# Kernel optimization log

Measured on AMD Instinct MI355X. Metric: run time of the kernel, lower is better.

## Reference

```python
import jax, jax.numpy as jnp
import numpy as np


def setup_inputs() -> dict:
    key = jax.random.key(0)
    ks = jax.random.split(key, 6)
    B, Lq, Lk, D = 8, 2048, 2048, 128
    return {
        "query": jax.random.normal(ks[0], (B, Lq, D), dtype=jnp.float32),
        "x": jax.random.normal(ks[1], (B, Lk, D), dtype=jnp.float32),
        "valid": jax.random.randint(ks[2], (B, Lq, Lk), 0, 2, dtype=jnp.int32),
        "Wq": jax.random.normal(ks[3], (D, D), dtype=jnp.float32) * 0.05,
        "Wk": jax.random.normal(ks[4], (D, D), dtype=jnp.float32) * 0.05,
        "Wv": jax.random.normal(ks[5], (D, D), dtype=jnp.float32) * 0.05,
    }


def reference(query, x, valid, Wq, Wk, Wv):
    # bias-free linear projections; torch Linear weight is [out, in] -> y = x @ W.T
    q = jnp.einsum("bqd,ad->bqa", query, Wq)   # [B, Lq, D]
    k = jnp.einsum("bkd,ad->bka", x, Wk)        # [B, Lk, D]
    v = jnp.einsum("bkd,ad->bka", x, Wv)        # [B, Lk, D]
    # scores (no scale arg passed in this config)
    att = jnp.einsum("bqd,bkd->bqk", q, k)      # [B, Lq, Lk]
    # max-subtraction BEFORE masking (matches original op order)
    att = att - jnp.max(att, axis=-1, keepdims=True)
    att = jnp.where(valid <= 0, -jnp.inf, att)
    att_w = jax.nn.softmax(att, axis=-1)
    # rows with all entries masked produce NaN -> fill with 0
    att_w = jnp.where(jnp.isnan(att_w), jnp.zeros_like(att_w), att_w)
    result = jnp.einsum("bqk,bkd->bqd", att_w, v)
    return (result, att_w)
```

## Files before the change

kernel.cpp:

```cpp
#include <hip/hip_runtime.h>
#include <float.h>
#include <math.h>


#define BB 8
#define LQ 2048
#define LK 2048
#define DD 128
#define NROWS (BB*LQ)
#define KS 4

typedef __attribute__((ext_vector_type(8))) _Float16 half8;
typedef __attribute__((ext_vector_type(8))) unsigned short ushort8;
typedef __attribute__((ext_vector_type(4))) float f32x4;

#define QH_OFF  (0u)
#define QL_OFF  (1u*NROWS*DD*2u)
#define KH_OFF  (2u*NROWS*DD*2u)
#define KL_OFF  (3u*NROWS*DD*2u)
#define VTH_OFF (4u*NROWS*DD*2u)
#define VTL_OFF (5u*NROWS*DD*2u)
#define BM_OFF  (6u*NROWS*DD*2u)
#define MZ_OFF  (BM_OFF + (unsigned)NROWS*(LK/8))

__device__ __forceinline__ f32x4 mfma16(half8 a, half8 b, f32x4 c) {
  return __builtin_amdgcn_mfma_f32_16x16x32_f16(a, b, c, 0, 0, 0);
}

__global__ __launch_bounds__(256, 3) void proj_kernel(
    const float* __restrict__ query, const float* __restrict__ x,
    const float* __restrict__ Wq, const float* __restrict__ Wk,
    const float* __restrict__ Wv, unsigned char* __restrict__ wsb)
{
  __shared__ float SB[8704];
  const int which = blockIdx.y;
  const float* __restrict__ src = (which == 0) ? query : x;
  const float* __restrict__ W   = (which == 0) ? Wq : (which == 1 ? Wk : Wv);
  const int t = threadIdx.x, l = t & 63, wv = t >> 6;
  const int lr = l & 15, lg = l >> 4;
  const int r0 = blockIdx.x * 64;

#pragma unroll
  for (int j = 0; j < 8; ++j) {
    const int flat = j * 1024 + t * 4;
    const int row = flat >> 7, col = flat & 127;
    *(float4*)&SB[row * 132 + col] = *(const float4*)&src[(size_t)(r0 + row) * DD + col];
  }
  __syncthreads();

  half8 ah[4], al[4];
#pragma unroll
  for (int dc = 0; dc < 4; ++dc) {
    const int base = (wv * 16 + lr) * 132 + dc * 32 + lg * 8;
    float4 f0 = *(const float4*)&SB[base];
    float4 f1 = *(const float4*)&SB[base + 4];
    float f[8] = {f0.x, f0.y, f0.z, f0.w, f1.x, f1.y, f1.z, f1.w};
#pragma unroll
    for (int e = 0; e < 8; ++e) {
      _Float16 h = (_Float16)f[e];
      ah[dc][e] = h;
      al[dc][e] = (_Float16)(f[e] - (float)h);
    }
  }
  __syncthreads();

  f32x4 acc[8];
#pragma unroll
  for (int a = 0; a < 8; ++a) acc[a] = (f32x4){0.f, 0.f, 0.f, 0.f};

#pragma unroll
  for (int dc = 0; dc < 4; ++dc) {
#pragma unroll
    for (int a = 0; a < 8; ++a) {
      const float* p = W + (size_t)(a * 16 + lr) * DD + dc * 32 + lg * 8;
      float4 f0 = *(const float4*)p;
      float4 f1 = *(const float4*)(p + 4);
      float f[8] = {f0.x, f0.y, f0.z, f0.w, f1.x, f1.y, f1.z, f1.w};
      half8 bh, bl;
#pragma unroll
      for (int e = 0; e < 8; ++e) {
        _Float16 h = (_Float16)f[e];
        bh[e] = h;
        bl[e] = (_Float16)(f[e] - (float)h);
      }
      acc[a] = mfma16(ah[dc], bh, acc[a]);
      acc[a] = mfma16(al[dc], bh, acc[a]);
      acc[a] = mfma16(ah[dc], bl, acc[a]);
    }
  }

  if (which < 2) {
    _Float16* Oh = (_Float16*)(wsb + (which == 0 ? QH_OFF : KH_OFF));
    _Float16* Ol = (_Float16*)(wsb + (which == 0 ? QL_OFF : KL_OFF));
#pragma unroll
    for (int a = 0; a < 8; ++a)
#pragma unroll
      for (int i = 0; i < 4; ++i) {
        const int ro = r0 + wv * 16 + lg * 4 + i;
        const int co = a * 16 + lr;
        float v = acc[a][i];
        _Float16 h = (_Float16)v;
        Oh[(size_t)ro * DD + co] = h;
        Ol[(size_t)ro * DD + co] = (_Float16)(v - (float)h);
      }
  } else {
    _Float16* TH = (_Float16*)SB;
    _Float16* TL = TH + 8704;
#pragma unroll
    for (int a = 0; a < 8; ++a)
#pragma unroll
      for (int i = 0; i < 4; ++i) {
        const int rl = wv * 16 + lg * 4 + i;
        const int co = a * 16 + lr;
        float v = acc[a][i];
        _Float16 h = (_Float16)v;
        TH[co * 68 + rl] = h;
        TL[co * 68 + rl] = (_Float16)(v - (float)h);
      }
    __syncthreads();
    _Float16* Vh = (_Float16*)(wsb + VTH_OFF);
    _Float16* Vl = (_Float16*)(wsb + VTL_OFF);
    const int b = r0 >> 11, kloc = r0 & 2047;
    const int d = t >> 1, hh = t & 1;
    const size_t gb = ((size_t)(b * DD + d)) * LK + kloc + hh * 32;
#pragma unroll
    for (int j = 0; j < 8; ++j) {
      *(ushort4*)(Vh + gb + j * 4) = *(const ushort4*)&TH[d * 68 + hh * 32 + j * 4];
      *(ushort4*)(Vl + gb + j * 4) = *(const ushort4*)&TL[d * 68 + hh * 32 + j * 4];
    }
  }
}

__global__ __launch_bounds__(256) void maskpack_kernel(
    const int* __restrict__ valid, unsigned long long* __restrict__ bm)
{
  const int t = threadIdx.x, l = t & 63, wv = t >> 6;
  const size_t base = (size_t)blockIdx.x * 32768 + (size_t)wv * 8192;
  for (int it = 0; it < 32; ++it) {
    int v0 = valid[base + (size_t)(it * 4 + 0) * 64 + l];
    int v1 = valid[base + (size_t)(it * 4 + 1) * 64 + l];
    int v2 = valid[base + (size_t)(it * 4 + 2) * 64 + l];
    int v3 = valid[base + (size_t)(it * 4 + 3) * 64 + l];
    unsigned long long m0 = __ballot(v0 > 0);
    unsigned long long m1 = __ballot(v1 > 0);
    unsigned long long m2 = __ballot(v2 > 0);
    unsigned long long m3 = __ballot(v3 > 0);
    if (l == 0) {
      bm[(base >> 6) + it * 4 + 0] = m0;
      bm[(base >> 6) + it * 4 + 1] = m1;
      bm[(base >> 6) + it * 4 + 2] = m2;
      bm[(base >> 6) + it * 4 + 3] = m3;
    }
  }
}

__global__ __launch_bounds__(256, 4) void scores_kernel(
    const unsigned char* __restrict__ wsb, float* __restrict__ att)
{
  __shared__ unsigned short KHs[64 * 136];
  __shared__ unsigned short KLs[64 * 136];
  const int t = threadIdx.x, l = t & 63, wv = t >> 6;
  const int lr = l & 15, lg = l >> 4;
  const int qb = blockIdx.x, b = blockIdx.y, ks = blockIdx.z;
  const int rowg = b * LQ + qb * 64;
  const int kbase = ks * 512;
  const _Float16* QH = (const _Float16*)(wsb + QH_OFF);
  const _Float16* QL = (const _Float16*)(wsb + QL_OFF);
  const _Float16* KH = (const _Float16*)(wsb + KH_OFF);
  const _Float16* KL = (const _Float16*)(wsb + KL_OFF);
  const unsigned* bm32 = (const unsigned*)(wsb + BM_OFF);
  float* M = (float*)(wsb + MZ_OFF);
  float* Z = M + KS * NROWS;

  half8 qh[4], ql[4];
#pragma unroll
  for (int dc = 0; dc < 4; ++dc) {
    const size_t idx = ((size_t)(rowg + wv * 16 + lr)) * DD + dc * 32 + lg * 8;
    qh[dc] = *(const half8*)(QH + idx);
    ql[dc] = *(const half8*)(QL + idx);
  }

  ushort8 rh[4], rl[4];
  auto issue_stage = [&](int kt) {
#pragma unroll
    for (int j = 0; j < 4; ++j) {
      const int flat = j * 2048 + t * 8;
      const int row = flat >> 7, col = flat & 127;
      const size_t g = ((size_t)(b * LK + kbase + kt * 64 + row)) * DD + col;
      rh[j] = *(const ushort8*)(KH + g);
      rl[j] = *(const ushort8*)(KL + g);
    }
  };
  auto write_stage = [&]() {
#pragma unroll
    for (int j = 0; j < 4; ++j) {
      const int flat = j * 2048 + t * 8;
      const int row = flat >> 7, col = flat & 127;
      *(ushort8*)&KHs[row * 136 + col] = rh[j];
      *(ushort8*)&KLs[row * 136 + col] = rl[j];
    }
  };

  issue_stage(0);
  write_stage();

  float m_run[4], z_run[4];
#pragma unroll
  for (int i = 0; i < 4; ++i) { m_run[i] = -FLT_MAX; z_run[i] = 0.f; }

  for (int kt = 0; kt < 8; ++kt) {
    const int k0 = kbase + kt * 64;
    if (kt < 7) issue_stage(kt + 1);
    unsigned mw0[4], mw1[4];
#pragma unroll
    for (int i = 0; i < 4; ++i) {
      uint2 u = *(const uint2*)(bm32 + ((size_t)(rowg + wv * 16 + lg * 4 + i)) * 64 + (k0 >> 5));
      mw0[i] = u.x; mw1[i] = u.y;
    }
    __syncthreads();

    f32x4 acc[4];
#pragma unroll
    for (int kg = 0; kg < 4; ++kg) acc[kg] = (f32x4){0.f, 0.f, 0.f, 0.f};
#pragma unroll
    for (int kg = 0; kg < 4; ++kg)
#pragma unroll
      for (int dc = 0; dc < 4; ++dc) {
        half8 bh = *(const half8*)&KHs[(kg * 16 + lr) * 136 + dc * 32 + lg * 8];
        half8 bl = *(const half8*)&KLs[(kg * 16 + lr) * 136 + dc * 32 + lg * 8];
        acc[kg] = mfma16(qh[dc], bh, acc[kg]);
        acc[kg] = mfma16(ql[dc], bh, acc[kg]);
        acc[kg] = mfma16(qh[dc], bl, acc[kg]);
      }

#pragma unroll
    for (int i = 0; i < 4; ++i) {
      float sv[4];
      float* ap = att + ((size_t)(rowg + wv * 16 + lg * 4 + i)) * LK + k0 + lr;
#pragma unroll
      for (int kg = 0; kg < 4; ++kg) {
        unsigned w = (kg < 2) ? mw0[i] : mw1[i];
        int bit = (w >> (((kg & 1) * 16) + lr)) & 1;
        float v = bit ? acc[kg][i] : -INFINITY;
        sv[kg] = v;
        ap[kg * 16] = v;
      }
      float tm = fmaxf(fmaxf(sv[0], sv[1]), fmaxf(sv[2], sv[3]));
#pragma unroll
      for (int o = 1; o < 16; o <<= 1) tm = fmaxf(tm, __shfl_xor(tm, o));
      const float mo = m_run[i], mn = fmaxf(mo, tm);
      float za = __expf(sv[0] - mn) + __expf(sv[1] - mn) +
                 __expf(sv[2] - mn) + __expf(sv[3] - mn);
      z_run[i] = z_run[i] * __expf(mo - mn) + za;
      m_run[i] = mn;
    }
    __syncthreads();
    if (kt < 7) write_stage();
  }

#pragma unroll
  for (int i = 0; i < 4; ++i) {
    float z = z_run[i];
#pragma unroll
    for (int o = 1; o < 16; o <<= 1) z += __shfl_xor(z, o);
    if (lr == 0) {
      const size_t row = (size_t)(rowg + wv * 16 + lg * 4 + i);
      M[(size_t)ks * NROWS + row] = m_run[i];
      Z[(size_t)ks * NROWS + row] = z;
    }
  }
}

__global__ __launch_bounds__(256, 3) void pv_kernel(
    const unsigned char* __restrict__ wsb, float* __restrict__ att,
    float* __restrict__ res)
{
  __shared__ float Ws[64 * 68];
  __shared__ unsigned short VHs[128 * 72];
  __shared__ unsigned short VLs[128 * 72];
  const int t = threadIdx.x, l = t & 63, wv = t >> 6;
  const int lr = l & 15, lg = l >> 4;
  const int qb = blockIdx.x, b = blockIdx.y, kp = blockIdx.z;
  const int rowg = b * LQ + qb * 64;
  const int kbase = kp * 512;
  const _Float16* VTH = (const _Float16*)(wsb + VTH_OFF);
  const _Float16* VTL = (const _Float16*)(wsb + VTL_OFF);
  const float* M = (const float*)(wsb + MZ_OFF);
  const float* Z = M + KS * NROWS;

  const int srow = t >> 2, scb = (t & 3) * 16;
  float mg, zi;
  {
    const size_t row = (size_t)(rowg + srow);
    float m0 = M[row], m1 = M[NROWS + row], m2 = M[2 * NROWS + row], m3 = M[3 * NROWS + row];
    mg = fmaxf(fmaxf(m0, m1), fmaxf(m2, m3));
    float z = Z[row] * __expf(m0 - mg) + Z[NROWS + row] * __expf(m1 - mg) +
              Z[2 * NROWS + row] * __expf(m2 - mg) + Z[3 * NROWS + row] * __expf(m3 - mg);
    zi = (z > 0.f) ? 1.f / z : 0.f;
  }

  ushort8 vhr[4], vlr[4];
  float4 sr[4];
  auto issue_V = [&](int kt) {
#pragma unroll
    for (int j = 0; j < 4; ++j) {
      const int flat = j * 2048 + t * 8;
      const int d = flat >> 6, kk = flat & 63;
      const size_t g = ((size_t)(b * DD + d)) * LK + kbase + kt * 64 + kk;
      vhr[j] = *(const ushort8*)(VTH + g);
      vlr[j] = *(const ushort8*)(VTL + g);
    }
  };
  auto issue_S = [&](int kt) {
    const size_t rb = (size_t)(rowg + srow) * LK + kbase + kt * 64 + scb;
#pragma unroll
    for (int j = 0; j < 4; ++j) sr[j] = *(const float4*)&att[rb + j * 4];
  };
  auto wcompute_write = [&](int kt) {
    const size_t rb = (size_t)(rowg + srow) * LK + kbase + kt * 64 + scb;
#pragma unroll
    for (int j = 0; j < 4; ++j) {
      float4 w4;
      w4.x = __expf(sr[j].x - mg) * zi;
      w4.y = __expf(sr[j].y - mg) * zi;
      w4.z = __expf(sr[j].z - mg) * zi;
      w4.w = __expf(sr[j].w - mg) * zi;
      *(float4*)&Ws[srow * 68 + scb + j * 4] = w4;
      *(float4*)&att[rb + j * 4] = w4;
    }
#pragma unroll
    for (int j = 0; j < 4; ++j) {
      const int flat = j * 2048 + t * 8;
      const int d = flat >> 6, kk = flat & 63;
      *(ushort8*)&VHs[d * 72 + kk] = vhr[j];
      *(ushort8*)&VLs[d * 72 + kk] = vlr[j];
    }
  };

  f32x4 oacc[8];
#pragma unroll
  for (int df = 0; df < 8; ++df) oacc[df] = (f32x4){0.f, 0.f, 0.f, 0.f};

  issue_V(0); issue_S(0);
  wcompute_write(0);

  for (int kt = 0; kt < 8; ++kt) {
    if (kt < 7) { issue_V(kt + 1); issue_S(kt + 1); }
    __syncthreads();

#pragma unroll
    for (int kc = 0; kc < 2; ++kc) {
      const int abase = (wv * 16 + lr) * 68 + kc * 32 + lg * 8;
      float4 a0 = *(const float4*)&Ws[abase];
      float4 a1 = *(const float4*)&Ws[abase + 4];
      half8 wf;
      wf[0] = (_Float16)a0.x; wf[1] = (_Float16)a0.y;
      wf[2] = (_Float16)a0.z; wf[3] = (_Float16)a0.w;
      wf[4] = (_Float16)a1.x; wf[5] = (_Float16)a1.y;
      wf[6] = (_Float16)a1.z; wf[7] = (_Float16)a1.w;
#pragma unroll
      for (int df = 0; df < 8; ++df) {
        half8 vh = *(const half8*)&VHs[(df * 16 + lr) * 72 + kc * 32 + lg * 8];
        half8 vl = *(const half8*)&VLs[(df * 16 + lr) * 72 + kc * 32 + lg * 8];
        oacc[df] = mfma16(wf, vh, oacc[df]);
        oacc[df] = mfma16(wf, vl, oacc[df]);
      }
    }
    __syncthreads();
    if (kt < 7) wcompute_write(kt + 1);
  }

#pragma unroll
  for (int df = 0; df < 8; ++df)
#pragma unroll
    for (int i = 0; i < 4; ++i)
      atomicAdd(&res[((size_t)(rowg + wv * 16 + lg * 4 + i)) * DD + df * 16 + lr],
                oacc[df][i]);
}

extern "C" void kernel_launch(void* const* d_in, const int* in_sizes, int n_in,
                              void* d_out, int out_size, void* d_ws, size_t ws_size,
                              hipStream_t stream)
{
  (void)in_sizes; (void)n_in; (void)out_size; (void)ws_size;
  const float* query = (const float*)d_in[0];
  const float* x     = (const float*)d_in[1];
  const int*   valid = (const int*)d_in[2];
  const float* Wq    = (const float*)d_in[3];
  const float* Wk    = (const float*)d_in[4];
  const float* Wv    = (const float*)d_in[5];

  float* out = (float*)d_out;
  float* res = out;
  float* att = out + (size_t)NROWS * DD;
  unsigned char* wsb = (unsigned char*)d_ws;

  hipMemsetAsync(res, 0, (size_t)NROWS * DD * sizeof(float), stream);
  proj_kernel<<<dim3(NROWS / 64, 3), 256, 0, stream>>>(query, x, Wq, Wk, Wv, wsb);
  maskpack_kernel<<<dim3(1024), 256, 0, stream>>>(
      valid, (unsigned long long*)(wsb + BM_OFF));
  scores_kernel<<<dim3(LQ / 64, BB, KS), 256, 0, stream>>>(wsb, att);
  pv_kernel<<<dim3(LQ / 64, BB, KS), 256, 0, stream>>>(wsb, att, res);
}
```

Before: 428.2 us.

## Drop V low-half split in PV, store weights as fp16, swizzle LDS tiles

The PV kernel no longer loads or multiplies the low-order fp16 half of V, which halves its V traffic and MFMA count. It converts softmax weights to fp16 once at staging time instead of on every read. K, V and the weight tiles in LDS move from padded layouts to XOR-swizzled unpadded layouts, which cuts LDS footprint and lets PV occupancy rise to 4 blocks. The cost is lower precision in the result, because V is now carried only as a single fp16 value, and the barrier placement is reordered.

```diff
diff --git a/kernel.cpp b/kernel.cpp
--- a/kernel.cpp
+++ b/kernel.cpp
@@ -11,7 +11,6 @@
 #define KS 4
 
 typedef __attribute__((ext_vector_type(8))) _Float16 half8;
-typedef __attribute__((ext_vector_type(8))) unsigned short ushort8;
 typedef __attribute__((ext_vector_type(4))) float f32x4;
 
 #define QH_OFF  (0u)
@@ -157,8 +156,8 @@
 __global__ __launch_bounds__(256, 4) void scores_kernel(
     const unsigned char* __restrict__ wsb, float* __restrict__ att)
 {
-  __shared__ unsigned short KHs[64 * 136];
-  __shared__ unsigned short KLs[64 * 136];
+  __shared__ _Float16 KHs[64 * 128];
+  __shared__ _Float16 KLs[64 * 128];
   const int t = threadIdx.x, l = t & 63, wv = t >> 6;
   const int lr = l & 15, lg = l >> 4;
   const int qb = blockIdx.x, b = blockIdx.y, ks = blockIdx.z;
@@ -180,24 +179,25 @@
     ql[dc] = *(const half8*)(QL + idx);
   }
 
-  ushort8 rh[4], rl[4];
+  half8 rh[4], rl[4];
   auto issue_stage = [&](int kt) {
 #pragma unroll
     for (int j = 0; j < 4; ++j) {
       const int flat = j * 2048 + t * 8;
       const int row = flat >> 7, col = flat & 127;
       const size_t g = ((size_t)(b * LK + kbase + kt * 64 + row)) * DD + col;
-      rh[j] = *(const ushort8*)(KH + g);
-      rl[j] = *(const ushort8*)(KL + g);
+      rh[j] = *(const half8*)(KH + g);
+      rl[j] = *(const half8*)(KL + g);
     }
   };
   auto write_stage = [&]() {
 #pragma unroll
     for (int j = 0; j < 4; ++j) {
       const int flat = j * 2048 + t * 8;
-      const int row = flat >> 7, col = flat & 127;
-      *(ushort8*)&KHs[row * 136 + col] = rh[j];
-      *(ushort8*)&KLs[row * 136 + col] = rl[j];
+      const int row = flat >> 7, c8 = (flat >> 3) & 15;
+      const int c8s = (c8 & 8) | ((c8 ^ row) & 7);
+      *(half8*)&KHs[row * 128 + c8s * 8] = rh[j];
+      *(half8*)&KLs[row * 128 + c8s * 8] = rl[j];
     }
   };
 
@@ -226,8 +226,10 @@
     for (int kg = 0; kg < 4; ++kg)
 #pragma unroll
       for (int dc = 0; dc < 4; ++dc) {
-        half8 bh = *(const half8*)&KHs[(kg * 16 + lr) * 136 + dc * 32 + lg * 8];
-        half8 bl = *(const half8*)&KLs[(kg * 16 + lr) * 136 + dc * 32 + lg * 8];
+        const int c8 = dc * 4 + lg;
+        const int c8s = (c8 & 8) | ((c8 ^ lr) & 7);
+        half8 bh = *(const half8*)&KHs[(kg * 16 + lr) * 128 + c8s * 8];
+        half8 bl = *(const half8*)&KLs[(kg * 16 + lr) * 128 + c8s * 8];
         acc[kg] = mfma16(qh[dc], bh, acc[kg]);
         acc[kg] = mfma16(ql[dc], bh, acc[kg]);
         acc[kg] = mfma16(qh[dc], bl, acc[kg]);
@@ -271,20 +273,18 @@
   }
 }
 
-__global__ __launch_bounds__(256, 3) void pv_kernel(
+__global__ __launch_bounds__(256, 4) void pv_kernel(
     const unsigned char* __restrict__ wsb, float* __restrict__ att,
     float* __restrict__ res)
 {
-  __shared__ float Ws[64 * 68];
-  __shared__ unsigned short VHs[128 * 72];
-  __shared__ unsigned short VLs[128 * 72];
+  __shared__ _Float16 VHs[128 * 64];
+  __shared__ _Float16 Wt[64 * 64];
   const int t = threadIdx.x, l = t & 63, wv = t >> 6;
   const int lr = l & 15, lg = l >> 4;
   const int qb = blockIdx.x, b = blockIdx.y, kp = blockIdx.z;
   const int rowg = b * LQ + qb * 64;
   const int kbase = kp * 512;
   const _Float16* VTH = (const _Float16*)(wsb + VTH_OFF);
-  const _Float16* VTL = (const _Float16*)(wsb + VTL_OFF);
   const float* M = (const float*)(wsb + MZ_OFF);
   const float* Z = M + KS * NROWS;
 
@@ -299,16 +299,14 @@
     zi = (z > 0.f) ? 1.f / z : 0.f;
   }
 
-  ushort8 vhr[4], vlr[4];
+  half8 vhr[4];
   float4 sr[4];
   auto issue_V = [&](int kt) {
 #pragma unroll
     for (int j = 0; j < 4; ++j) {
       const int flat = j * 2048 + t * 8;
       const int d = flat >> 6, kk = flat & 63;
-      const size_t g = ((size_t)(b * DD + d)) * LK + kbase + kt * 64 + kk;
-      vhr[j] = *(const ushort8*)(VTH + g);
-      vlr[j] = *(const ushort8*)(VTL + g);
+      vhr[j] = *(const half8*)(VTH + ((size_t)(b * DD + d)) * LK + kbase + kt * 64 + kk);
     }
   };
   auto issue_S = [&](int kt) {
@@ -316,8 +314,9 @@
 #pragma unroll
     for (int j = 0; j < 4; ++j) sr[j] = *(const float4*)&att[rb + j * 4];
   };
-  auto wcompute_write = [&](int kt) {
+  auto w_stage = [&](int kt) {
     const size_t rb = (size_t)(rowg + srow) * LK + kbase + kt * 64 + scb;
+    float wf[16];
 #pragma unroll
     for (int j = 0; j < 4; ++j) {
       float4 w4;
@@ -325,15 +324,21 @@
       w4.y = __expf(sr[j].y - mg) * zi;
       w4.z = __expf(sr[j].z - mg) * zi;
       w4.w = __expf(sr[j].w - mg) * zi;
-      *(float4*)&Ws[srow * 68 + scb + j * 4] = w4;
       *(float4*)&att[rb + j * 4] = w4;
-    }
+      wf[j * 4 + 0] = w4.x; wf[j * 4 + 1] = w4.y;
+      wf[j * 4 + 2] = w4.z; wf[j * 4 + 3] = w4.w;
+    }
+    half8 h0, h1;
+#pragma unroll
+    for (int e = 0; e < 8; ++e) { h0[e] = (_Float16)wf[e]; h1[e] = (_Float16)wf[8 + e]; }
+    const int g0 = (t & 3) * 2;
+    *(half8*)&Wt[srow * 64 + (((g0)     ^ srow) & 7) * 8] = h0;
+    *(half8*)&Wt[srow * 64 + (((g0 + 1) ^ srow) & 7) * 8] = h1;
 #pragma unroll
     for (int j = 0; j < 4; ++j) {
       const int flat = j * 2048 + t * 8;
-      const int d = flat >> 6, kk = flat & 63;
-      *(ushort8*)&VHs[d * 72 + kk] = vhr[j];
-      *(ushort8*)&VLs[d * 72 + kk] = vlr[j];
+      const int d = flat >> 6, c8 = (flat >> 3) & 7;
+      *(half8*)&VHs[d * 64 + ((c8 ^ d) & 7) * 8] = vhr[j];
     }
   };
 
@@ -342,32 +347,27 @@
   for (int df = 0; df < 8; ++df) oacc[df] = (f32x4){0.f, 0.f, 0.f, 0.f};
 
   issue_V(0); issue_S(0);
-  wcompute_write(0);
+  w_stage(0);
+  __syncthreads();
 
   for (int kt = 0; kt < 8; ++kt) {
     if (kt < 7) { issue_V(kt + 1); issue_S(kt + 1); }
+
+#pragma unroll
+    for (int kc = 0; kc < 2; ++kc) {
+      const int c8 = kc * 4 + lg;
+      half8 wfr = *(const half8*)&Wt[(wv * 16 + lr) * 64 + ((c8 ^ (lr & 7)) & 7) * 8];
+#pragma unroll
+      for (int df = 0; df < 8; ++df) {
+        half8 vh = *(const half8*)&VHs[(df * 16 + lr) * 64 + ((c8 ^ (lr & 7)) & 7) * 8];
+        oacc[df] = mfma16(wfr, vh, oacc[df]);
+      }
+    }
     __syncthreads();
-
-#pragma unroll
-    for (int kc = 0; kc < 2; ++kc) {
-      const int abase = (wv * 16 + lr) * 68 + kc * 32 + lg * 8;
-      float4 a0 = *(const float4*)&Ws[abase];
-      float4 a1 = *(const float4*)&Ws[abase + 4];
-      half8 wf;
-      wf[0] = (_Float16)a0.x; wf[1] = (_Float16)a0.y;
-      wf[2] = (_Float16)a0.z; wf[3] = (_Float16)a0.w;
-      wf[4] = (_Float16)a1.x; wf[5] = (_Float16)a1.y;
-      wf[6] = (_Float16)a1.z; wf[7] = (_Float16)a1.w;
-#pragma unroll
-      for (int df = 0; df < 8; ++df) {
-        half8 vh = *(const half8*)&VHs[(df * 16 + lr) * 72 + kc * 32 + lg * 8];
-        half8 vl = *(const half8*)&VLs[(df * 16 + lr) * 72 + kc * 32 + lg * 8];
-        oacc[df] = mfma16(wf, vh, oacc[df]);
-        oacc[df] = mfma16(wf, vl, oacc[df]);
-      }
-    }
-    __syncthreads();
-    if (kt < 7) wcompute_write(kt + 1);
+    if (kt < 7) {
+      w_stage(kt + 1);
+      __syncthreads();
+    }
   }
 
 #pragma unroll
```

After: 416.7 us. 1.03x faster.
